# Performance work log

Hardware: AMD Instinct MI355X
Metric: run time of the kernel (lower is better)

The kernel has to match this reference:

```python
import jax, jax.numpy as jnp
import numpy as np
from jax import lax

B = 64          # batch
IMG = 384       # image H=W
PATCH = 16      # stem patch size -> 24x24 grid
C = 192         # hidden_channels
K = 5           # knn_graph k (hard-coded in extract_graph)
HG = IMG // PATCH
N = HG * HG     # total_num_nodes = 576
HID = 4 * C     # FFN expansion
PRED_HID = 1024
NUM_CLASSES = 1


def setup_inputs() -> dict:
    key = jax.random.key(0)
    ks = jax.random.split(key, 16)
    def w(k, shape, s=0.02):
        return jax.random.normal(k, shape, jnp.float32) * s
    f32 = jnp.float32
    return {
        "x": jax.random.normal(ks[0], (B, 3, IMG, IMG), f32),
        # stem: 16x16 patch-embed conv
        "stem_w": w(ks[1], (C, 3, PATCH, PATCH)),
        "stem_b": jnp.zeros((C,), f32),
        "pos_embed": w(ks[2], (1, C, HG, HG)),
        # GSAT edge-attention MLP: concat(src,dst) -> C -> 1 -> sigmoid
        "att_w1": w(ks[3], (2 * C, C)), "att_b1": jnp.zeros((C,), f32),
        "att_w2": w(ks[4], (C, 1)),     "att_b2": jnp.zeros((1,), f32),
        # two message-passing layers (GIN-style update)
        "gnn_w1": w(ks[5], (C, C)), "gnn_b1": jnp.zeros((C,), f32),
        "gnn_w2": w(ks[6], (C, C)), "gnn_b2": jnp.zeros((C,), f32),
        # FFN (1x1 convs == channel matmuls), BN in eval mode (mean0/var1)
        "ffn_w1": w(ks[7], (C, HID)), "ffn_b1": jnp.zeros((HID,), f32),
        "ffn_g1": jnp.ones((HID,), f32), "ffn_be1": jnp.zeros((HID,), f32),
        "ffn_w2": w(ks[8], (HID, C)), "ffn_b2": jnp.zeros((C,), f32),
        "ffn_g2": jnp.ones((C,), f32), "ffn_be2": jnp.zeros((C,), f32),
        # prediction head: 1x1 conv C->1024, BN(eval), gelu, 1x1 conv 1024->num_classes
        "pred_w1": w(ks[9], (C, PRED_HID)), "pred_b1": jnp.zeros((PRED_HID,), f32),
        "pred_g": jnp.ones((PRED_HID,), f32), "pred_be": jnp.zeros((PRED_HID,), f32),
        "pred_w2": w(ks[10], (PRED_HID, NUM_CLASSES)), "pred_b2": jnp.zeros((NUM_CLASSES,), f32),
    }


def reference(x, stem_w, stem_b, pos_embed,
              att_w1, att_b1, att_w2, att_b2,
              gnn_w1, gnn_b1, gnn_w2, gnn_b2,
              ffn_w1, ffn_b1, ffn_g1, ffn_be1,
              ffn_w2, ffn_b2, ffn_g2, ffn_be2,
              pred_w1, pred_b1, pred_g, pred_be, pred_w2, pred_b2):
    # ---- stem + pos_embed ----
    feat = lax.conv_general_dilated(x, stem_w, (PATCH, PATCH), 'VALID',
                                    dimension_numbers=('NCHW', 'OIHW', 'NCHW'))
    feat = feat + stem_b[None, :, None, None] + pos_embed        # [B,C,Hg,Wg]
    b, c, hg, wg = feat.shape
    n = hg * wg
    nf = feat.reshape(b, c, n).transpose(0, 2, 1)                # [B,N,C]
    nfd = lax.stop_gradient(nf)                                  # extract_graph under no_grad

    # ---- kNN graph build: per-image pairwise sq. distances + top-k ----
    sq = jnp.sum(nfd * nfd, axis=-1)                             # [B,N]
    d2 = sq[:, :, None] + sq[:, None, :] - 2.0 * jnp.einsum('bnc,bmc->bnm', nfd, nfd)
    d2 = d2 + jnp.eye(n, dtype=d2.dtype) * 1e9                   # exclude self-loops
    _, idx = lax.top_k(-d2, K)                                   # [B,N,K] nearest neighbors
    src = (idx + (jnp.arange(b) * n)[:, None, None]).reshape(-1)  # [E] global neighbor idx
    dst = jnp.repeat(jnp.arange(b * n), K)                        # [E] global center idx

    # ---- GSAT GNN: edge attention + attention-weighted message passing ----
    h = nfd.reshape(b * n, c)                                    # [BN,C] (detached)
    e = jax.nn.relu(jnp.concatenate([h[src], h[dst]], axis=-1) @ att_w1 + att_b1)
    edge_att = jax.nn.sigmoid(e @ att_w2 + att_b2)               # [E,1]
    for Wg, bg in ((gnn_w1, gnn_b1), (gnn_w2, gnn_b2)):
        m = jax.ops.segment_sum(edge_att * h[src], dst, num_segments=b * n)
        h = jax.nn.relu((h + m) @ Wg + bg)                       # GIN-style update

    # ---- FFN (1x1 convs) with residual, BN eval-mode affine ----
    t = h.reshape(b, n, c)                                       # [B,N,C]
    u = jax.nn.gelu((t @ ffn_w1 + ffn_b1) * ffn_g1 + ffn_be1, approximate=False)
    t = t + ((u @ ffn_w2 + ffn_b2) * ffn_g2 + ffn_be2)

    # ---- global average pool + prediction head ----
    g = jnp.mean(t, axis=1)                                      # [B,C]
    p = jax.nn.gelu((g @ pred_w1 + pred_b1) * pred_g + pred_be, approximate=False)
    prediction = p @ pred_w2 + pred_b2                           # [B,num_classes]
    return edge_att, prediction
```

## Files before the change

### kernel.cpp

```cpp
#include <hip/hip_runtime.h>
#include <hip/hip_bf16.h>
#include <math.h>

constexpr int B_    = 64;
constexpr int C_    = 192;
constexpr int N_    = 576;
constexpr int BN_   = B_ * N_;
constexpr int K_    = 5;
constexpr int E_    = BN_ * K_;

__device__ __forceinline__ float gelu_exact(float x) {
    return 0.5f * x * (1.0f + erff(x * 0.70710678118654752440f));
}

__device__ __forceinline__ float bf2f(unsigned short v) {
    return __uint_as_float(((unsigned)v) << 16);
}
__device__ __forceinline__ unsigned short f2bf(float x) {
    __hip_bfloat16 h = __float2bfloat16(x);
    return *(unsigned short*)&h;
}

__global__ __launch_bounds__(256) void prep_all_k(
    const float* __restrict__ stem_w, const float* __restrict__ gnn_w1,
    const float* __restrict__ gnn_w2, const float* __restrict__ ffn_w1,
    const float* __restrict__ ffn_w2, const float* __restrict__ att_w1,
    float* __restrict__ wt, unsigned short* __restrict__ wg1T,
    unsigned short* __restrict__ wg2T, unsigned short* __restrict__ wf1T,
    unsigned short* __restrict__ wf2T, unsigned short* __restrict__ waHi,
    unsigned short* __restrict__ waLo)
{
    int gid = blockIdx.x * 256 + threadIdx.x;
    if (gid < 147456) {
        int k = gid / 192, oc = gid % 192;
        wt[gid] = stem_w[oc * 768 + k];
    } else if (gid < 184320) {
        int g = gid - 147456;
        int n = g / 192, k = g % 192;
        wg1T[g] = f2bf(gnn_w1[(size_t)k * 192 + n]);
    } else if (gid < 221184) {
        int g = gid - 184320;
        int n = g / 192, k = g % 192;
        wg2T[g] = f2bf(gnn_w2[(size_t)k * 192 + n]);
    } else if (gid < 368640) {
        int g = gid - 221184;
        int n = g / 192, k = g % 192;
        wf1T[g] = f2bf(ffn_w1[(size_t)k * 768 + n]);
    } else if (gid < 516096) {
        int g = gid - 368640;
        int n = g / 768, k = g % 768;
        wf2T[g] = f2bf(ffn_w2[(size_t)k * 192 + n]);
    } else {
        int g = gid - 516096;
        int half = g / 36864, r = g % 36864;
        int n = r / 192, k = r % 192;
        float v = att_w1[(size_t)(half * 192 + k) * 192 + n];
        unsigned short h = f2bf(v);
        waHi[g] = h;
        waLo[g] = f2bf(v - bf2f(h));
    }
}

__global__ __launch_bounds__(256) void stem_gemm96f_k(
    const float* __restrict__ x, const float* __restrict__ Wt,
    const float* __restrict__ sb, const float* __restrict__ pos,
    float* __restrict__ nf, float* __restrict__ nfT,
    unsigned short* __restrict__ ahi, unsigned short* __restrict__ alo)
{
    __shared__ float As[96][68];
    __shared__ float Ws[64][68];
    const int tid = threadIdx.x;
    const int tr = tid >> 4, tc = tid & 15;
    const int mb = blockIdx.x;
    const int nb = blockIdx.y;
    const int b  = mb / 6;
    const int n0 = (mb % 6) * 96;

    float4 acc[6];
    #pragma unroll
    for (int i = 0; i < 6; ++i) acc[i] = float4{0.f, 0.f, 0.f, 0.f};

    for (int kc = 0; kc < 768; kc += 64) {
        #pragma unroll
        for (int i = 0; i < 6; ++i) {
            int q = i * 256 + tid;
            int m = q >> 4, kq = q & 15;
            int k = kc + kq * 4;
            int ci = k >> 8, rem = k & 255, dy = rem >> 4, dx = rem & 15;
            int n = n0 + m, py = n / 24, px = n % 24;
            const float* src = &x[(((size_t)(b * 3 + ci) * 384) + py * 16 + dy) * 384
                                  + px * 16 + dx];
            *(float4*)&As[m][kq * 4] = *(const float4*)src;
        }
        #pragma unroll
        for (int i = 0; i < 4; ++i) {
            int q = i * 256 + tid;
            int m = q >> 4, kq = q & 15;
            *(float4*)&Ws[m][kq * 4] =
                *(const float4*)&Wt[(size_t)(kc + m) * 192 + nb * 64 + kq * 4];
        }
        __syncthreads();
        #pragma unroll
        for (int k4 = 0; k4 < 64; k4 += 4) {
            float4 a4[6], b4[4];
            #pragma unroll
            for (int i = 0; i < 6; ++i) a4[i] = *(const float4*)&As[tr * 6 + i][k4];
            #pragma unroll
            for (int kk = 0; kk < 4; ++kk) b4[kk] = *(const float4*)&Ws[k4 + kk][tc * 4];
            #pragma unroll
            for (int i = 0; i < 6; ++i) {
                const float av[4] = {a4[i].x, a4[i].y, a4[i].z, a4[i].w};
                #pragma unroll
                for (int kk = 0; kk < 4; ++kk) {
                    acc[i].x += av[kk] * b4[kk].x;
                    acc[i].y += av[kk] * b4[kk].y;
                    acc[i].z += av[kk] * b4[kk].z;
                    acc[i].w += av[kk] * b4[kk].w;
                }
            }
        }
        __syncthreads();
    }

    #pragma unroll
    for (int i = 0; i < 6; ++i) {
        int n = n0 + tr * 6 + i;
        int row = b * 576 + n;
        int oc0 = nb * 64 + tc * 4;
        float v[4] = {acc[i].x, acc[i].y, acc[i].z, acc[i].w};
        unsigned short hv[4], lv[4];
        #pragma unroll
        for (int j = 0; j < 4; ++j) {
            int oc = oc0 + j;
            v[j] = v[j] + sb[oc] + pos[oc * 576 + n];
            nfT[((size_t)(b * 192 + oc)) * 576 + n] = v[j];
            hv[j] = f2bf(v[j]);
            lv[j] = f2bf(v[j] - bf2f(hv[j]));
        }
        *(float4*)&nf[(size_t)row * 192 + oc0] = float4{v[0], v[1], v[2], v[3]};
        *(ushort4*)&ahi[(size_t)row * 192 + oc0] = ushort4{hv[0], hv[1], hv[2], hv[3]};
        *(ushort4*)&alo[(size_t)row * 192 + oc0] = ushort4{lv[0], lv[1], lv[2], lv[3]};
    }
}

__global__ __launch_bounds__(256) void sq_k(const float* __restrict__ nf,
                                            float* __restrict__ sq) {
    int wid = threadIdx.x >> 6, lane = threadIdx.x & 63;
    int n = blockIdx.x * 4 + wid;
    const float* row = nf + (size_t)n * 192;
    float s = 0.f;
    #pragma unroll
    for (int c = 0; c < 3; ++c) { float v = row[lane + c * 64]; s += v * v; }
    #pragma unroll
    for (int off = 32; off; off >>= 1) s += __shfl_down(s, off);
    if (lane == 0) sq[n] = s;
}

__global__ __launch_bounds__(64) void knn_sym_k(
    const float* __restrict__ nfT, const float* __restrict__ sqn,
    float* __restrict__ candV, int* __restrict__ candI)
{
    __shared__ float smem[64 * 69];
    float* As  = smem;
    float* Bs  = smem + 2048;
    float* d2s = smem;

    const int tid = threadIdx.x;
    const int tr = tid >> 3, tc = tid & 7;
    const int b = blockIdx.y;
    int t = blockIdx.x;
    int bi = 0;
    while (t >= 9 - bi) { t -= 9 - bi; ++bi; }
    const int bj = bi + t;
    const int r0 = bi * 64, c0 = bj * 64;

    float acc[8][8];
    #pragma unroll
    for (int i = 0; i < 8; ++i)
        #pragma unroll
        for (int j = 0; j < 8; ++j) acc[i][j] = 0.f;

    for (int kc = 0; kc < 192; kc += 32) {
        #pragma unroll
        for (int i = 0; i < 8; ++i) {
            int q = i * 64 + tid;
            int k = q >> 4, c4 = (q & 15) * 4;
            const float* srow = &nfT[((size_t)(b * 192 + kc + k)) * 576];
            *(float4*)&As[k * 64 + c4] = *(const float4*)&srow[r0 + c4];
            *(float4*)&Bs[k * 64 + c4] = *(const float4*)&srow[c0 + c4];
        }
        __syncthreads();
        #pragma unroll 8
        for (int kk = 0; kk < 32; ++kk) {
            float4 a0 = *(const float4*)&As[kk * 64 + tr * 8];
            float4 a1 = *(const float4*)&As[kk * 64 + tr * 8 + 4];
            float4 b0 = *(const float4*)&Bs[kk * 64 + tc * 8];
            float4 b1 = *(const float4*)&Bs[kk * 64 + tc * 8 + 4];
            const float av[8] = {a0.x, a0.y, a0.z, a0.w, a1.x, a1.y, a1.z, a1.w};
            const float bv[8] = {b0.x, b0.y, b0.z, b0.w, b1.x, b1.y, b1.z, b1.w};
            #pragma unroll
            for (int i = 0; i < 8; ++i)
                #pragma unroll
                for (int j = 0; j < 8; ++j)
                    acc[i][j] += av[i] * bv[j];
        }
        __syncthreads();
    }

    #pragma unroll
    for (int i = 0; i < 8; ++i) {
        int rl = tr * 8 + i, rg = r0 + rl;
        float sr = sqn[b * 576 + rg];
        #pragma unroll
        for (int j = 0; j < 8; ++j) {
            int cl = tc * 8 + j, cg = c0 + cl;
            float d = sr + sqn[b * 576 + cg] - 2.f * acc[i][j];
            if (cg == rg) d += 1e9f;
            d2s[rl * 69 + cl] = d;
        }
    }
    __syncthreads();

    {
        const int r = tid;
        float tv[5]; int ti[5];
        #pragma unroll
        for (int p = 0; p < 5; ++p) { tv[p] = 3.4e38f; ti[p] = 0; }
        for (int c = 0; c < 64; ++c) {
            float cv = d2s[r * 69 + c];
            if (cv < tv[4]) {
                int ci = c0 + c;
                #pragma unroll
                for (int q = 0; q < 5; ++q) {
                    bool less = cv < tv[q];
                    float nv = less ? tv[q] : cv;
                    int ni   = less ? ti[q] : ci;
                    tv[q] = less ? cv : tv[q];
                    ti[q] = less ? ci : ti[q];
                    cv = nv; ci = ni;
                }
            }
        }
        int gr = b * 576 + r0 + r;
        #pragma unroll
        for (int p = 0; p < 5; ++p) {
            candV[(size_t)gr * 45 + bj * 5 + p] = tv[p];
            candI[(size_t)gr * 45 + bj * 5 + p] = ti[p];
        }
    }

    if (bi != bj) {
        const int c = tid;
        float tv[5]; int ti[5];
        #pragma unroll
        for (int p = 0; p < 5; ++p) { tv[p] = 3.4e38f; ti[p] = 0; }
        for (int r = 0; r < 64; ++r) {
            float cv = d2s[r * 69 + c];
            if (cv < tv[4]) {
                int ci = r0 + r;
                #pragma unroll
                for (int q = 0; q < 5; ++q) {
                    bool less = cv < tv[q];
                    float nv = less ? tv[q] : cv;
                    int ni   = less ? ti[q] : ci;
                    tv[q] = less ? cv : tv[q];
                    ti[q] = less ? ci : ti[q];
                    cv = nv; ci = ni;
                }
            }
        }
        int gr = b * 576 + c0 + c;
        #pragma unroll
        for (int p = 0; p < 5; ++p) {
            candV[(size_t)gr * 45 + bi * 5 + p] = tv[p];
            candI[(size_t)gr * 45 + bi * 5 + p] = ti[p];
        }
    }
}

__global__ __launch_bounds__(256) void knn_merge_k(
    const float* __restrict__ candV, const int* __restrict__ candI,
    int* __restrict__ idxOut)
{
    int r = blockIdx.x * 256 + threadIdx.x;
    float tv[5]; int ti[5];
    #pragma unroll
    for (int p = 0; p < 5; ++p) { tv[p] = 3.4e38f; ti[p] = 0; }
    #pragma unroll 5
    for (int s = 0; s < 45; ++s) {
        float cv = candV[(size_t)r * 45 + s];
        if (cv < tv[4]) {
            int cidx = candI[(size_t)r * 45 + s];
            #pragma unroll
            for (int q = 0; q < 5; ++q) {
                bool less = cv < tv[q];
                float nv = less ? tv[q] : cv;
                int ni   = less ? ti[q] : cidx;
                tv[q] = less ? cv : tv[q];
                ti[q] = less ? cidx : ti[q];
                cv = nv; cidx = ni;
            }
        }
    }
    int base = (r / 576) * 576;
    #pragma unroll
    for (int p = 0; p < 5; ++p) idxOut[r * 5 + p] = base + ti[p];
}

template <int EPI>
__global__ __launch_bounds__(256) void gemm_rm_k(
    const float* __restrict__ A, const float* __restrict__ W, float* __restrict__ out,
    int M, int N, int K,
    const float* __restrict__ bias, const float* __restrict__ gsc,
    const float* __restrict__ gsh, const float* __restrict__ res)
{
    __shared__ float As[64][68];
    __shared__ float Ws[64][68];
    const int tid = threadIdx.x;
    const int tr = tid >> 4, tc = tid & 15;
    const int mBase = blockIdx.x * 64, nBase = blockIdx.y * 64;

    float4 acc[4];
    acc[0] = acc[1] = acc[2] = acc[3] = float4{0.f, 0.f, 0.f, 0.f};

    for (int kc = 0; kc < K; kc += 64) {
        #pragma unroll
        for (int i = 0; i < 4; ++i) {
            int q = i * 256 + tid;
            int m = q >> 4, kq = q & 15;
            *(float4*)&As[m][kq * 4] =
                *(const float4*)&A[(size_t)(mBase + m) * K + kc + kq * 4];
            *(float4*)&Ws[m][kq * 4] =
                *(const float4*)&W[(size_t)(kc + m) * N + nBase + kq * 4];
        }
        __syncthreads();
        #pragma unroll
        for (int k4 = 0; k4 < 64; k4 += 4) {
            float4 a4[4], b4[4];
            #pragma unroll
            for (int i = 0; i < 4; ++i) a4[i] = *(const float4*)&As[tr * 4 + i][k4];
            #pragma unroll
            for (int kk = 0; kk < 4; ++kk) b4[kk] = *(const float4*)&Ws[k4 + kk][tc * 4];
            #pragma unroll
            for (int i = 0; i < 4; ++i) {
                const float av[4] = {a4[i].x, a4[i].y, a4[i].z, a4[i].w};
                #pragma unroll
                for (int kk = 0; kk < 4; ++kk) {
                    acc[i].x += av[kk] * b4[kk].x;
                    acc[i].y += av[kk] * b4[kk].y;
                    acc[i].z += av[kk] * b4[kk].z;
                    acc[i].w += av[kk] * b4[kk].w;
                }
            }
        }
        __syncthreads();
    }

    #pragma unroll
    for (int i = 0; i < 4; ++i) {
        int row = mBase + tr * 4 + i;
        int n0 = nBase + tc * 4;
        float v[4] = {acc[i].x, acc[i].y, acc[i].z, acc[i].w};
        #pragma unroll
        for (int j = 0; j < 4; ++j) {
            int n = n0 + j;
            float xv = v[j];
            if (EPI == 1) xv += bias[n];
            if (EPI == 2) { xv += bias[n]; xv = fmaxf(xv, 0.f); }
            if (EPI == 3) { xv = (xv + bias[n]) * gsc[n] + gsh[n]; xv = gelu_exact(xv); }
            if (EPI == 4) {
                xv = res[(size_t)row * N + n] + (xv + bias[n]) * gsc[n] + gsh[n];
            }
            v[j] = xv;
        }
        *(float4*)&out[(size_t)row * N + n0] = float4{v[0], v[1], v[2], v[3]};
    }
}

template <int EPI>
__global__ __launch_bounds__(256) void gemm_mfma_k(
    const unsigned short* __restrict__ A, const unsigned short* __restrict__ Bt,
    unsigned short* __restrict__ out, int M, int N, int K,
    const float* __restrict__ bias, const float* __restrict__ gsc,
    const float* __restrict__ gsh, const unsigned short* __restrict__ res)
{
    using frag = __attribute__((ext_vector_type(8))) short;
    using facc = __attribute__((ext_vector_type(4))) float;
    __shared__ unsigned short As[256][72];
    __shared__ unsigned short Bs[64][72];
    const int tid = threadIdx.x;
    const int wave = tid >> 6, lane = tid & 63;
    const int m16 = lane & 15, quad = lane >> 4;
    const int mBase = blockIdx.x * 256, nBase = blockIdx.y * 64;

    facc zero = {0.f, 0.f, 0.f, 0.f};
    facc acc[4][4];
    #pragma unroll
    for (int ms = 0; ms < 4; ++ms)
        #pragma unroll
        for (int t = 0; t < 4; ++t) acc[ms][t] = zero;

    for (int kc = 0; kc < K; kc += 64) {
        #pragma unroll
        for (int r = 0; r < 8; ++r) {
            int q = r * 256 + tid;
            int row = q >> 3, c8 = (q & 7) * 8;
            *(int4*)&As[row][c8] =
                *(const int4*)&A[(size_t)(mBase + row) * K + kc + c8];
        }
        #pragma unroll
        for (int r = 0; r < 2; ++r) {
            int q = r * 256 + tid;
            int row = q >> 3, c8 = (q & 7) * 8;
            *(int4*)&Bs[row][c8] =
                *(const int4*)&Bt[(size_t)(nBase + row) * K + kc + c8];
        }
        __syncthreads();
        #pragma unroll
        for (int kk = 0; kk < 64; kk += 32) {
            frag bfr[4];
            #pragma unroll
            for (int t = 0; t < 4; ++t)
                bfr[t] = *(const frag*)&Bs[t * 16 + m16][kk + quad * 8];
            #pragma unroll
            for (int ms = 0; ms < 4; ++ms) {
                frag a = *(const frag*)&As[64 * wave + ms * 16 + m16][kk + quad * 8];
                #pragma unroll
                for (int t = 0; t < 4; ++t)
                    acc[ms][t] = __builtin_amdgcn_mfma_f32_16x16x32_bf16(a, bfr[t], acc[ms][t], 0, 0, 0);
            }
        }
        __syncthreads();
    }

    #pragma unroll
    for (int ms = 0; ms < 4; ++ms) {
        #pragma unroll
        for (int t = 0; t < 4; ++t) {
            #pragma unroll
            for (int r = 0; r < 4; ++r) {
                int row = mBase + 64 * wave + ms * 16 + quad * 4 + r;
                int col = nBase + t * 16 + m16;
                float xv = acc[ms][t][r];
                if (EPI == 2) { xv += bias[col]; xv = fmaxf(xv, 0.f); }
                if (EPI == 3) { xv = (xv + bias[col]) * gsc[col] + gsh[col]; xv = gelu_exact(xv); }
                if (EPI == 4) {
                    xv = bf2f(res[(size_t)row * N + col]) + (xv + bias[col]) * gsc[col] + gsh[col];
                }
                out[(size_t)row * N + col] = f2bf(xv);
            }
        }
    }
}

template <int EPI>
__global__ __launch_bounds__(256) void gemm_mfma_split_k(
    const unsigned short* __restrict__ Ah, const unsigned short* __restrict__ Al,
    const unsigned short* __restrict__ Bh, const unsigned short* __restrict__ Bl,
    float* __restrict__ out, int M, int N, int K, const float* __restrict__ bias)
{
    using frag = __attribute__((ext_vector_type(8))) short;
    using facc = __attribute__((ext_vector_type(4))) float;
    __shared__ unsigned short AsH[64][72], AsL[64][72];
    __shared__ unsigned short BsH[64][72], BsL[64][72];
    const int tid = threadIdx.x;
    const int wave = tid >> 6, lane = tid & 63;
    const int m16 = lane & 15, quad = lane >> 4;
    const int mBase = blockIdx.x * 64, nBase = blockIdx.y * 64;

    facc zero = {0.f, 0.f, 0.f, 0.f};
    facc acc[4];
    #pragma unroll
    for (int t = 0; t < 4; ++t) acc[t] = zero;

    for (int kc = 0; kc < K; kc += 64) {
        #pragma unroll
        for (int r = 0; r < 2; ++r) {
            int q = r * 256 + tid;
            int row = q >> 3, c8 = (q & 7) * 8;
            *(int4*)&AsH[row][c8] = *(const int4*)&Ah[(size_t)(mBase + row) * K + kc + c8];
            *(int4*)&AsL[row][c8] = *(const int4*)&Al[(size_t)(mBase + row) * K + kc + c8];
            *(int4*)&BsH[row][c8] = *(const int4*)&Bh[(size_t)(nBase + row) * K + kc + c8];
            *(int4*)&BsL[row][c8] = *(const int4*)&Bl[(size_t)(nBase + row) * K + kc + c8];
        }
        __syncthreads();
        #pragma unroll
        for (int kk = 0; kk < 64; kk += 32) {
            frag ah = *(const frag*)&AsH[16 * wave + m16][kk + quad * 8];
            frag al = *(const frag*)&AsL[16 * wave + m16][kk + quad * 8];
            #pragma unroll
            for (int t = 0; t < 4; ++t) {
                frag bh = *(const frag*)&BsH[t * 16 + m16][kk + quad * 8];
                frag bl = *(const frag*)&BsL[t * 16 + m16][kk + quad * 8];
                acc[t] = __builtin_amdgcn_mfma_f32_16x16x32_bf16(ah, bh, acc[t], 0, 0, 0);
                acc[t] = __builtin_amdgcn_mfma_f32_16x16x32_bf16(ah, bl, acc[t], 0, 0, 0);
                acc[t] = __builtin_amdgcn_mfma_f32_16x16x32_bf16(al, bh, acc[t], 0, 0, 0);
            }
        }
        __syncthreads();
    }

    #pragma unroll
    for (int t = 0; t < 4; ++t) {
        #pragma unroll
        for (int r = 0; r < 4; ++r) {
            int row = mBase + 16 * wave + quad * 4 + r;
            int col = nBase + t * 16 + m16;
            float xv = acc[t][r];
            if (EPI == 1) xv += bias[col];
            out[(size_t)row * N + col] = xv;
        }
    }
}

__global__ __launch_bounds__(256) void edge_att_k(
    const float* __restrict__ hA, const float* __restrict__ hB,
    const int* __restrict__ idx, const float* __restrict__ w2,
    const float* __restrict__ b2, float* __restrict__ att)
{
    int wid = threadIdx.x >> 6, lane = threadIdx.x & 63;
    int e = blockIdx.x * 4 + wid;
    int dst = e / K_;
    int src = idx[e];
    float s = 0.f;
    #pragma unroll
    for (int c0 = 0; c0 < 3; ++c0) {
        int c = lane + c0 * 64;
        float v = hA[(size_t)src * 192 + c] + hB[(size_t)dst * 192 + c];
        v = fmaxf(v, 0.f);
        s += v * w2[c];
    }
    #pragma unroll
    for (int off = 32; off; off >>= 1) s += __shfl_down(s, off);
    if (lane == 0) att[e] = 1.f / (1.f + expf(-(s + b2[0])));
}

__device__ __forceinline__ float ldv(const float* p, size_t i) { return p[i]; }
__device__ __forceinline__ float ldv(const unsigned short* p, size_t i) { return bf2f(p[i]); }

template <typename TI>
__global__ __launch_bounds__(256) void msg_bf_k(
    const TI* __restrict__ h, const float* __restrict__ att,
    const int* __restrict__ idx, unsigned short* __restrict__ s)
{
    int g = blockIdx.x * 256 + threadIdx.x;
    int n = g / 192, c = g % 192;
    float acc = ldv(h, (size_t)g);
    #pragma unroll
    for (int p = 0; p < K_; ++p) {
        int sp = idx[n * K_ + p];
        acc += att[n * K_ + p] * ldv(h, (size_t)sp * 192 + c);
    }
    s[g] = f2bf(acc);
}

__global__ void pool_bf16_k(const unsigned short* __restrict__ t, float* __restrict__ g) {
    int b = blockIdx.x, c = threadIdx.x;
    float s = 0.f;
    for (int n = 0; n < 576; ++n) s += bf2f(t[((size_t)b * 576 + n) * 192 + c]);
    g[b * 192 + c] = s * (1.f / 576.f);
}

__global__ __launch_bounds__(256) void head2_k(
    const float* __restrict__ p, const float* __restrict__ w2,
    const float* __restrict__ b2, float* __restrict__ out)
{
    int b = blockIdx.x;
    float s = 0.f;
    for (int j = threadIdx.x; j < 1024; j += 256) s += p[(size_t)b * 1024 + j] * w2[j];
    #pragma unroll
    for (int off = 32; off; off >>= 1) s += __shfl_down(s, off);
    __shared__ float ls[4];
    int wid = threadIdx.x >> 6, lane = threadIdx.x & 63;
    if (lane == 0) ls[wid] = s;
    __syncthreads();
    if (threadIdx.x == 0) out[b] = ls[0] + ls[1] + ls[2] + ls[3] + b2[0];
}

extern "C" void kernel_launch(void* const* d_in, const int* in_sizes, int n_in,
                              void* d_out, int out_size, void* d_ws, size_t ws_size,
                              hipStream_t stream) {
    const float* x        = (const float*)d_in[0];
    const float* stem_w   = (const float*)d_in[1];
    const float* stem_b   = (const float*)d_in[2];
    const float* pos      = (const float*)d_in[3];
    const float* att_w1   = (const float*)d_in[4];
    const float* att_b1   = (const float*)d_in[5];
    const float* att_w2   = (const float*)d_in[6];
    const float* att_b2   = (const float*)d_in[7];
    const float* gnn_w1   = (const float*)d_in[8];
    const float* gnn_b1   = (const float*)d_in[9];
    const float* gnn_w2   = (const float*)d_in[10];
    const float* gnn_b2   = (const float*)d_in[11];
    const float* ffn_w1   = (const float*)d_in[12];
    const float* ffn_b1   = (const float*)d_in[13];
    const float* ffn_g1   = (const float*)d_in[14];
    const float* ffn_be1  = (const float*)d_in[15];
    const float* ffn_w2   = (const float*)d_in[16];
    const float* ffn_b2   = (const float*)d_in[17];
    const float* ffn_g2   = (const float*)d_in[18];
    const float* ffn_be2  = (const float*)d_in[19];
    const float* pred_w1  = (const float*)d_in[20];
    const float* pred_b1  = (const float*)d_in[21];
    const float* pred_g   = (const float*)d_in[22];
    const float* pred_be  = (const float*)d_in[23];
    const float* pred_w2  = (const float*)d_in[24];
    const float* pred_b2  = (const float*)d_in[25];

    float* ws = (float*)d_ws;
    const size_t RSZ = (size_t)BN_ * C_;
    float* R0 = ws;
    float* R1 = R0 + RSZ;
    float* R2 = R1 + RSZ;
    float* R3 = R2 + RSZ;
    float* sqb = R3 + RSZ;
    int*   idxb = (int*)(sqb + BN_);
    float* gb = (float*)(idxb + E_);
    float* pb = gb + 64 * C_;
    unsigned short* wg1T = (unsigned short*)(pb + 64 * 1024);
    unsigned short* wg2T = wg1T + 192 * 192;
    unsigned short* wf1T = wg2T + 192 * 192;
    unsigned short* wf2T = wf1T + 768 * 192;
    unsigned short* waHi = wf2T + 192 * 768;
    unsigned short* waLo = waHi + 2 * 192 * 192;
    float* Wt = (float*)(waLo + 2 * 192 * 192);
    unsigned short* Ahi = (unsigned short*)(Wt + 768 * 192);
    unsigned short* Alo = Ahi + RSZ;

    float* candV = R1;
    int*   candI = (int*)(R1 + (size_t)BN_ * 45);

    unsigned short* Sb    = (unsigned short*)R1;
    unsigned short* Hb    = (unsigned short*)(R1 + RSZ / 2);
    unsigned short* Tb    = (unsigned short*)R2;
    unsigned short* ToutB = (unsigned short*)(R2 + RSZ / 2);
    unsigned short* Ub    = (unsigned short*)R3;

    float* att  = (float*)d_out;
    float* pred = att + E_;

    prep_all_k<<<2304, 256, 0, stream>>>(stem_w, gnn_w1, gnn_w2, ffn_w1,
        ffn_w2, att_w1, Wt, wg1T, wg2T, wf1T, wf2T, waHi, waLo);

    stem_gemm96f_k<<<dim3(384, 3), 256, 0, stream>>>(x, Wt, stem_b, pos,
        R0, R3, Ahi, Alo);

    sq_k<<<BN_ / 4, 256, 0, stream>>>(R0, sqb);
    knn_sym_k<<<dim3(45, 64), 64, 0, stream>>>(R3, sqb, candV, candI);
    knn_merge_k<<<BN_ / 256, 256, 0, stream>>>(candV, candI, idxb);

    gemm_mfma_split_k<0><<<dim3(576, 3), 256, 0, stream>>>(Ahi, Alo,
        waHi, waLo, R1, BN_, 192, 192, nullptr);
    gemm_mfma_split_k<1><<<dim3(576, 3), 256, 0, stream>>>(Ahi, Alo,
        waHi + 36864, waLo + 36864, R2, BN_, 192, 192, att_b1);
    edge_att_k<<<E_ / 4, 256, 0, stream>>>(R1, R2, idxb, att_w2, att_b2, att);

    msg_bf_k<float><<<BN_ * C_ / 256, 256, 0, stream>>>(R0, att, idxb, Sb);
    gemm_mfma_k<2><<<dim3(144, 3), 256, 0, stream>>>(Sb, wg1T, Hb,
        BN_, 192, 192, gnn_b1, nullptr, nullptr, nullptr);
    msg_bf_k<unsigned short><<<BN_ * C_ / 256, 256, 0, stream>>>(Hb, att, idxb, Sb);
    gemm_mfma_k<2><<<dim3(144, 3), 256, 0, stream>>>(Sb, wg2T, Tb,
        BN_, 192, 192, gnn_b2, nullptr, nullptr, nullptr);

    for (int ch = 0; ch < 2; ++ch) {
        const unsigned short* Ain = Tb + (size_t)ch * 18432 * 192;
        unsigned short* Tout = ToutB + (size_t)ch * 18432 * 192;
        gemm_mfma_k<3><<<dim3(72, 12), 256, 0, stream>>>(Ain, wf1T, Ub,
            18432, 768, 192, ffn_b1, ffn_g1, ffn_be1, nullptr);
        gemm_mfma_k<4><<<dim3(72, 3), 256, 0, stream>>>(Ub, wf2T, Tout,
            18432, 192, 768, ffn_b2, ffn_g2, ffn_be2, Ain);
    }

    pool_bf16_k<<<64, 192, 0, stream>>>(ToutB, gb);
    gemm_rm_k<3><<<dim3(1, 16), 256, 0, stream>>>(gb, pred_w1, pb,
        64, 1024, 192, pred_b1, pred_g, pred_be, nullptr);
    head2_k<<<64, 256, 0, stream>>>(pb, pred_w2, pred_b2, pred);
}
```

Baseline: 771.4 us.

## Move stem transpose to tiled kernel and enlarge split-GEMM M tile

Result: faster. 729.8 us (-5.4%).

```diff
diff --git a/kernel.cpp b/kernel.cpp
--- a/kernel.cpp
+++ b/kernel.cpp
@@ -61,10 +61,10 @@
     }
 }
 
-__global__ __launch_bounds__(256) void stem_gemm96f_k(
+__global__ __launch_bounds__(256) void stem_gemm96a_k(
     const float* __restrict__ x, const float* __restrict__ Wt,
     const float* __restrict__ sb, const float* __restrict__ pos,
-    float* __restrict__ nf, float* __restrict__ nfT,
+    float* __restrict__ nf,
     unsigned short* __restrict__ ahi, unsigned short* __restrict__ alo)
 {
     __shared__ float As[96][68];
@@ -133,13 +133,30 @@
         for (int j = 0; j < 4; ++j) {
             int oc = oc0 + j;
             v[j] = v[j] + sb[oc] + pos[oc * 576 + n];
-            nfT[((size_t)(b * 192 + oc)) * 576 + n] = v[j];
             hv[j] = f2bf(v[j]);
             lv[j] = f2bf(v[j] - bf2f(hv[j]));
         }
         *(float4*)&nf[(size_t)row * 192 + oc0] = float4{v[0], v[1], v[2], v[3]};
         *(ushort4*)&ahi[(size_t)row * 192 + oc0] = ushort4{hv[0], hv[1], hv[2], hv[3]};
         *(ushort4*)&alo[(size_t)row * 192 + oc0] = ushort4{lv[0], lv[1], lv[2], lv[3]};
+    }
+}
+
+__global__ void transpose_nf_k(const float* __restrict__ nf, float* __restrict__ nfT) {
+    __shared__ float tile[32][33];
+    int b = blockIdx.z;
+    int n0 = blockIdx.x * 32, c0 = blockIdx.y * 32;
+    int tx = threadIdx.x, ty = threadIdx.y;
+    #pragma unroll
+    for (int r = 0; r < 4; ++r) {
+        int i = ty * 4 + r;
+        tile[i][tx] = nf[((size_t)b * 576 + n0 + i) * 192 + c0 + tx];
+    }
+    __syncthreads();
+    #pragma unroll
+    for (int r = 0; r < 4; ++r) {
+        int i = ty * 4 + r;
+        nfT[((size_t)b * 192 + c0 + i) * 576 + n0 + tx] = tile[tx][i];
     }
 }
 
@@ -461,54 +478,71 @@
 {
     using frag = __attribute__((ext_vector_type(8))) short;
     using facc = __attribute__((ext_vector_type(4))) float;
-    __shared__ unsigned short AsH[64][72], AsL[64][72];
-    __shared__ unsigned short BsH[64][72], BsL[64][72];
+    __shared__ unsigned short AsH[128][72], AsL[128][72];
+    __shared__ unsigned short BsH[64][72],  BsL[64][72];
     const int tid = threadIdx.x;
     const int wave = tid >> 6, lane = tid & 63;
     const int m16 = lane & 15, quad = lane >> 4;
-    const int mBase = blockIdx.x * 64, nBase = blockIdx.y * 64;
+    const int mBase = blockIdx.x * 128, nBase = blockIdx.y * 64;
 
     facc zero = {0.f, 0.f, 0.f, 0.f};
-    facc acc[4];
-    #pragma unroll
-    for (int t = 0; t < 4; ++t) acc[t] = zero;
+    facc acc[2][4];
+    #pragma unroll
+    for (int ms = 0; ms < 2; ++ms)
+        #pragma unroll
+        for (int t = 0; t < 4; ++t) acc[ms][t] = zero;
 
     for (int kc = 0; kc < K; kc += 64) {
         #pragma unroll
-        for (int r = 0; r < 2; ++r) {
+        for (int r = 0; r < 4; ++r) {
             int q = r * 256 + tid;
             int row = q >> 3, c8 = (q & 7) * 8;
             *(int4*)&AsH[row][c8] = *(const int4*)&Ah[(size_t)(mBase + row) * K + kc + c8];
             *(int4*)&AsL[row][c8] = *(const int4*)&Al[(size_t)(mBase + row) * K + kc + c8];
+        }
+        #pragma unroll
+        for (int r = 0; r < 2; ++r) {
+            int q = r * 256 + tid;
+            int row = q >> 3, c8 = (q & 7) * 8;
             *(int4*)&BsH[row][c8] = *(const int4*)&Bh[(size_t)(nBase + row) * K + kc + c8];
             *(int4*)&BsL[row][c8] = *(const int4*)&Bl[(size_t)(nBase + row) * K + kc + c8];
         }
         __syncthreads();
         #pragma unroll
         for (int kk = 0; kk < 64; kk += 32) {
-            frag ah = *(const frag*)&AsH[16 * wave + m16][kk + quad * 8];
-            frag al = *(const frag*)&AsL[16 * wave + m16][kk + quad * 8];
+            frag bh[4], bl[4];
             #pragma unroll
             for (int t = 0; t < 4; ++t) {
-                frag bh = *(const frag*)&BsH[t * 16 + m16][kk + quad * 8];
-                frag bl = *(const frag*)&BsL[t * 16 + m16][kk + quad * 8];
-                acc[t] = __builtin_amdgcn_mfma_f32_16x16x32_bf16(ah, bh, acc[t], 0, 0, 0);
-                acc[t] = __builtin_amdgcn_mfma_f32_16x16x32_bf16(ah, bl, acc[t], 0, 0, 0);
-                acc[t] = __builtin_amdgcn_mfma_f32_16x16x32_bf16(al, bh, acc[t], 0, 0, 0);
-            }
-        }
-        __syncthreads();
-    }
-
-    #pragma unroll
-    for (int t = 0; t < 4; ++t) {
-        #pragma unroll
-        for (int r = 0; r < 4; ++r) {
-            int row = mBase + 16 * wave + quad * 4 + r;
-            int col = nBase + t * 16 + m16;
-            float xv = acc[t][r];
-            if (EPI == 1) xv += bias[col];
-            out[(size_t)row * N + col] = xv;
+                bh[t] = *(const frag*)&BsH[t * 16 + m16][kk + quad * 8];
+                bl[t] = *(const frag*)&BsL[t * 16 + m16][kk + quad * 8];
+            }
+            #pragma unroll
+            for (int ms = 0; ms < 2; ++ms) {
+                frag ah = *(const frag*)&AsH[32 * wave + ms * 16 + m16][kk + quad * 8];
+                frag al = *(const frag*)&AsL[32 * wave + ms * 16 + m16][kk + quad * 8];
+                #pragma unroll
+                for (int t = 0; t < 4; ++t) {
+                    acc[ms][t] = __builtin_amdgcn_mfma_f32_16x16x32_bf16(ah, bh[t], acc[ms][t], 0, 0, 0);
+                    acc[ms][t] = __builtin_amdgcn_mfma_f32_16x16x32_bf16(ah, bl[t], acc[ms][t], 0, 0, 0);
+                    acc[ms][t] = __builtin_amdgcn_mfma_f32_16x16x32_bf16(al, bh[t], acc[ms][t], 0, 0, 0);
+                }
+            }
+        }
+        __syncthreads();
+    }
+
+    #pragma unroll
+    for (int ms = 0; ms < 2; ++ms) {
+        #pragma unroll
+        for (int t = 0; t < 4; ++t) {
+            #pragma unroll
+            for (int r = 0; r < 4; ++r) {
+                int row = mBase + 32 * wave + ms * 16 + quad * 4 + r;
+                int col = nBase + t * 16 + m16;
+                float xv = acc[ms][t][r];
+                if (EPI == 1) xv += bias[col];
+                out[(size_t)row * N + col] = xv;
+            }
         }
     }
 }
@@ -642,16 +676,17 @@
     prep_all_k<<<2304, 256, 0, stream>>>(stem_w, gnn_w1, gnn_w2, ffn_w1,
         ffn_w2, att_w1, Wt, wg1T, wg2T, wf1T, wf2T, waHi, waLo);
 
-    stem_gemm96f_k<<<dim3(384, 3), 256, 0, stream>>>(x, Wt, stem_b, pos,
-        R0, R3, Ahi, Alo);
+    stem_gemm96a_k<<<dim3(384, 3), 256, 0, stream>>>(x, Wt, stem_b, pos,
+        R0, Ahi, Alo);
 
     sq_k<<<BN_ / 4, 256, 0, stream>>>(R0, sqb);
+    transpose_nf_k<<<dim3(18, 6, 64), dim3(32, 8), 0, stream>>>(R0, R3);
     knn_sym_k<<<dim3(45, 64), 64, 0, stream>>>(R3, sqb, candV, candI);
     knn_merge_k<<<BN_ / 256, 256, 0, stream>>>(candV, candI, idxb);
 
-    gemm_mfma_split_k<0><<<dim3(576, 3), 256, 0, stream>>>(Ahi, Alo,
+    gemm_mfma_split_k<0><<<dim3(288, 3), 256, 0, stream>>>(Ahi, Alo,
         waHi, waLo, R1, BN_, 192, 192, nullptr);
-    gemm_mfma_split_k<1><<<dim3(576, 3), 256, 0, stream>>>(Ahi, Alo,
+    gemm_mfma_split_k<1><<<dim3(288, 3), 256, 0, stream>>>(Ahi, Alo,
         waHi + 36864, waLo + 36864, R2, BN_, 192, 192, att_b1);
     edge_att_k<<<E_ / 4, 256, 0, stream>>>(R1, R2, idxb, att_w2, att_b2, att);
 
```
